# Kernel optimization log

Measured on AMD Instinct MI355X. Metric: run time of the kernel, lower is better.

## Reference

```python
import math
import jax, jax.numpy as jnp
import numpy as np

N_HEADS = 16


def setup_inputs() -> dict:
    key = jax.random.key(0)
    qkv = jax.random.normal(key, (4, 3072, 2048), dtype=jnp.float32)
    return {"qkv": qkv}


def reference(qkv) -> jnp.ndarray:
    bs, width, length = qkv.shape
    assert width % (3 * N_HEADS) == 0
    ch = width // (3 * N_HEADS)
    # [bs*H, 3*ch, T] -> q, k, v each [bs*H, ch, T]
    qkv_r = qkv.reshape(bs * N_HEADS, 3 * ch, length)
    q, k, v = qkv_r[:, :ch], qkv_r[:, ch:2 * ch], qkv_r[:, 2 * ch:]
    scale = 1.0 / math.sqrt(math.sqrt(ch))
    # scores: [bs*H, T, T]
    weight = jnp.einsum('bct,bcs->bts', q * scale, k * scale)
    weight = jax.nn.softmax(weight.astype(jnp.float32), axis=-1).astype(weight.dtype)
    a = jnp.einsum('bts,bcs->bct', weight, v)  # [bs*H, ch, T]
    return a.reshape(bs, N_HEADS * ch, length)
```

## Files before the change

kernel.cpp:

```cpp
#include <hip/hip_runtime.h>
#include <hip/hip_bf16.h>
#include <cstdint>
#include <cstddef>

typedef short bf16x8 __attribute__((ext_vector_type(8)));
typedef float f32x16 __attribute__((ext_vector_type(16)));
typedef unsigned int uint2v __attribute__((ext_vector_type(2)));

#define QSCALE 0.18033688011112043f

__device__ __forceinline__ short f2bf(float f) {
  union { __hip_bfloat16 b; short s; } u;
  u.b = __float2bfloat16(f);
  return u.s;
}

__device__ __forceinline__ float exp2v(float x) {
  float r;
  asm("v_exp_f32 %0, %1" : "=v"(r) : "v"(x));
  return r;
}

__device__ __forceinline__ unsigned int packbf2(float a, float b) {
  union { __hip_bfloat162 h; unsigned int w; } u;
  u.h = __float22bfloat162_rn(float2{a, b});
  return u.w;
}

__device__ __forceinline__ unsigned int fbits(float f) {
  union { float f; unsigned int u; } x; x.f = f; return x.u;
}
__device__ __forceinline__ float bfloat(unsigned int u) {
  union { unsigned int u; float f; } x; x.u = u; return x.f;
}

__device__ __forceinline__ float fmax_x32(float v) {
  const uint2v r = __builtin_amdgcn_permlane32_swap(fbits(v), fbits(v),
                                                    false, false);
  return fmaxf(bfloat(r[0]), bfloat(r[1]));
}
__device__ __forceinline__ float fadd_x32(float v) {
  const uint2v r = __builtin_amdgcn_permlane32_swap(fbits(v), fbits(v),
                                                    false, false);
  return bfloat(r[0]) + bfloat(r[1]);
}

__device__ __forceinline__ void gload16(const short* g, char* l) {
  __builtin_amdgcn_global_load_lds(
      (const __attribute__((address_space(1))) void*)g,
      (__attribute__((address_space(3))) void*)l, 16, 0, 0);
}

__global__ __launch_bounds__(256, 4) void qkv_prep_kernel(
    const float* __restrict__ qkv, short* __restrict__ Kt,
    short* __restrict__ Vb) {
  const int bh = blockIdx.x >> 5;
  const int s0 = (blockIdx.x & 31) << 6;
  const int tid = threadIdx.x;
  const int row = tid >> 2;
  const int part = tid & 3;
  __shared__ float lds[64 * 65];

  const size_t qb = (size_t)bh * (192 * 2048);

  {
    const float* src = qkv + qb + (size_t)(64 + row) * 2048 + s0 + part * 16;
#pragma unroll
    for (int k4 = 0; k4 < 4; ++k4) {
      float4 v = ((const float4*)src)[k4];
      float* p = &lds[row * 65 + part * 16 + k4 * 4];
      p[0] = v.x; p[1] = v.y; p[2] = v.z; p[3] = v.w;
    }
  }
  __syncthreads();
  {
    bf16x8 o0, o1;
#pragma unroll
    for (int k = 0; k < 8; ++k) o0[k] = f2bf(lds[(part * 16 + k) * 65 + row]);
#pragma unroll
    for (int k = 0; k < 8; ++k) o1[k] = f2bf(lds[(part * 16 + 8 + k) * 65 + row]);
    short* dst = Kt + ((size_t)bh * 2048 + s0 + row) * 64 + part * 16;
    *(bf16x8*)dst = o0;
    *(bf16x8*)(dst + 8) = o1;
  }
  {
    const float* src = qkv + qb + (size_t)(128 + row) * 2048 + s0 + part * 16;
    float a[16];
#pragma unroll
    for (int k4 = 0; k4 < 4; ++k4) {
      float4 v = ((const float4*)src)[k4];
      a[k4 * 4 + 0] = v.x; a[k4 * 4 + 1] = v.y;
      a[k4 * 4 + 2] = v.z; a[k4 * 4 + 3] = v.w;
    }
    bf16x8 o0, o1;
#pragma unroll
    for (int k = 0; k < 8; ++k) { o0[k] = f2bf(a[k]); o1[k] = f2bf(a[8 + k]); }
    short* dst = Vb + ((size_t)bh * 64 + row) * 2048 + s0 + part * 16;
    *(bf16x8*)dst = o0;
    *(bf16x8*)(dst + 8) = o1;
  }
}

__global__ __launch_bounds__(512, 4) void attn32_kernel(
    const float* __restrict__ qkv, const short* __restrict__ Kt,
    const short* __restrict__ Vb, float* __restrict__ out) {
  const int bid = blockIdx.x;
  const int vid = (bid & 7) * 64 + (bid >> 3);
  const int bh = vid >> 3;
  const int tblk = vid & 7;
  const int tid = threadIdx.x;
  const int wv = tid >> 6;
  const int lane = tid & 63;
  const int tl = lane & 31;
  const int hi = lane >> 5;
  const int t0w = tblk * 256 + wv * 32;

  __shared__ __align__(16) char smem[32768];

  const size_t qb = (size_t)bh * (192 * 2048);
  bf16x8 qf[4];
#pragma unroll
  for (int kc = 0; kc < 4; ++kc) {
#pragma unroll
    for (int j = 0; j < 8; ++j) {
      const int c = kc * 16 + hi * 8 + j;
      qf[kc][j] = f2bf(qkv[qb + (size_t)c * 2048 + t0w + tl] * QSCALE);
    }
  }

  f32x16 zv;
#pragma unroll
  for (int r = 0; r < 16; ++r) zv[r] = 0.f;

  f32x16 acc[2];
#pragma unroll
  for (int cb = 0; cb < 2; ++cb) acc[cb] = zv;

  float mrun = -1e30f;
  float lsum = 0.f;

  const int rsw = (tl & 7) * 16;
  int off[2][4];
#pragma unroll
  for (int x = 0; x < 2; ++x)
#pragma unroll
    for (int j = 0; j < 4; ++j)
      off[x][j] = (x * 32 + tl) * 128 + ((j * 32 + hi * 16) ^ rsw);

  const int srow = tid >> 3;
  const int sl = tid & 7;
  const short* kg = Kt + (size_t)bh * (2048 * 64) + (size_t)srow * 64 +
                    ((sl ^ (srow & 7)) * 8);
  const short* vg = Vb + ((size_t)bh * 64 + srow) * 2048 +
                    ((sl ^ (srow & 7)) * 8);
  const int ldb = wv * 1024;

  gload16(kg, smem + ldb);
  gload16(vg, smem + 8192 + ldb);

#pragma unroll 2
  for (int ch = 0; ch < 32; ++ch) {
    char* const Kls = smem + (ch & 1) * 16384;
    char* const Vls = Kls + 8192;

    __syncthreads();

    if (ch < 31) {
      char* const Knx = smem + ((ch + 1) & 1) * 16384;
      gload16(kg + (size_t)(ch + 1) * 4096, Knx + ldb);
      gload16(vg + (ch + 1) * 64, Knx + 8192 + ldb);
    }

    f32x16 lg[2];
#pragma unroll
    for (int st = 0; st < 2; ++st) {
      bf16x8 ka = *(const bf16x8*)(Kls + off[st][0]);
      lg[st] = __builtin_amdgcn_mfma_f32_32x32x16_bf16(ka, qf[0], zv, 0, 0, 0);
#pragma unroll
      for (int kc = 1; kc < 4; ++kc) {
        ka = *(const bf16x8*)(Kls + off[st][kc]);
        lg[st] = __builtin_amdgcn_mfma_f32_32x32x16_bf16(ka, qf[kc], lg[st],
                                                         0, 0, 0);
      }
    }

    float w[11];
#pragma unroll
    for (int i = 0; i < 5; ++i)
      w[i] = fmaxf(fmaxf(lg[0][3 * i], lg[0][3 * i + 1]), lg[0][3 * i + 2]);
    w[5] = fmaxf(fmaxf(lg[0][15], lg[1][0]), lg[1][1]);
#pragma unroll
    for (int i = 0; i < 4; ++i)
      w[6 + i] = fmaxf(fmaxf(lg[1][3 * i + 2], lg[1][3 * i + 3]),
                       lg[1][3 * i + 4]);
    w[10] = fmaxf(lg[1][14], lg[1][15]);
    const float x0 = fmaxf(fmaxf(w[0], w[1]), w[2]);
    const float x1 = fmaxf(fmaxf(w[3], w[4]), w[5]);
    const float x2 = fmaxf(fmaxf(w[6], w[7]), w[8]);
    const float x3 = fmaxf(w[9], w[10]);
    float cm = fmax_x32(fmaxf(fmaxf(x0, x1), fmaxf(x2, x3)));
    if (!__all(cm <= mrun + 8.0f)) {
      const float nm = fmaxf(mrun, cm);
      const float fac = exp2v(mrun - nm);
      mrun = nm;
      lsum *= fac;
#pragma unroll
      for (int cb = 0; cb < 2; ++cb)
#pragma unroll
        for (int r = 0; r < 16; ++r) acc[cb][r] *= fac;
    }

    float ps = 0.f;
#pragma unroll
    for (int st = 0; st < 2; ++st) {
#pragma unroll
      for (int r = 0; r < 16; ++r) lg[st][r] = exp2v(lg[st][r] - mrun);
#pragma unroll
      for (int r = 0; r < 8; ++r) ps += lg[st][2 * r] + lg[st][2 * r + 1];
    }
    lsum += ps;

    bf16x8 pa[4];
#pragma unroll
    for (int st = 0; st < 2; ++st) {
#pragma unroll
      for (int kl = 0; kl < 2; ++kl) {
        const unsigned int p0a = packbf2(lg[st][8 * kl + 0], lg[st][8 * kl + 1]);
        const unsigned int p0b = packbf2(lg[st][8 * kl + 2], lg[st][8 * kl + 3]);
        const unsigned int p1a = packbf2(lg[st][8 * kl + 4], lg[st][8 * kl + 5]);
        const unsigned int p1b = packbf2(lg[st][8 * kl + 6], lg[st][8 * kl + 7]);
        const unsigned int sa = hi ? p0a : p1a;
        const unsigned int sb = hi ? p0b : p1b;
        const unsigned int ra = __shfl_xor(sa, 32);
        const unsigned int rb = __shfl_xor(sb, 32);
        union { unsigned int w[4]; bf16x8 v; } u;
        u.w[0] = hi ? ra : p0a;
        u.w[1] = hi ? rb : p0b;
        u.w[2] = hi ? p1a : ra;
        u.w[3] = hi ? p1b : rb;
        pa[st * 2 + kl] = u.v;
      }
    }

#pragma unroll
    for (int cb = 0; cb < 2; ++cb) {
#pragma unroll
      for (int ks = 0; ks < 4; ++ks) {
        const bf16x8 vb = *(const bf16x8*)(Vls + off[cb][ks]);
        acc[cb] = __builtin_amdgcn_mfma_f32_32x32x16_bf16(vb, pa[ks], acc[cb],
                                                          0, 0, 0);
      }
    }
  }

  const float ls = fadd_x32(lsum);
  const float inv = 1.0f / ls;
#pragma unroll
  for (int cb = 0; cb < 2; ++cb) {
#pragma unroll
    for (int r = 0; r < 16; ++r) {
      const int c = cb * 32 + (r & 3) + 8 * (r >> 2) + 4 * hi;
      out[((size_t)bh * 64 + c) * 2048 + t0w + tl] = acc[cb][r] * inv;
    }
  }
}

extern "C" void kernel_launch(void* const* d_in, const int* in_sizes, int n_in,
                              void* d_out, int out_size, void* d_ws,
                              size_t ws_size, hipStream_t stream) {
  (void)in_sizes; (void)n_in; (void)out_size;
  const float* qkv = (const float*)d_in[0];
  float* out = (float*)d_out;
  const size_t kv_elems = (size_t)64 * 2048 * 64;
  if (ws_size < kv_elems * 2 * sizeof(short)) return;
  short* Kt = (short*)d_ws;
  short* Vb = Kt + kv_elems;
  hipLaunchKernelGGL(qkv_prep_kernel, dim3(2048), dim3(256), 0, stream,
                     qkv, Kt, Vb);
  hipLaunchKernelGGL(attn32_kernel, dim3(512), dim3(512), 0, stream,
                     qkv, Kt, Vb, out);
}
```

Baseline: 117.0 us.

## Split each key chunk across wave pairs and merge softmax partials in LDS

Each block now covers 128 query positions instead of 256, and the grid doubles to 1024 blocks. Within each 64-key chunk, a pair of waves splits the keys: each wave does one 32x32 score tile and half of the PV MFMAs. At the end, the two partial online-softmax states (max, sum, accumulator) are combined through LDS before the output is written. This gives more blocks and halves per-wave register state so occupancy can rise (launch bounds raised to 8). The cost is K/V loaded to LDS twice as often per query, plus an extra reduction and barrier in the epilogue.

Result: slower. 309.5 us (+164.6%).

```diff
diff --git a/kernel.cpp b/kernel.cpp
--- a/kernel.cpp
+++ b/kernel.cpp
@@ -101,21 +101,23 @@
   }
 }
 
-__global__ __launch_bounds__(512, 4) void attn32_kernel(
+__global__ __launch_bounds__(512, 8) void attn32_kernel(
     const float* __restrict__ qkv, const short* __restrict__ Kt,
     const short* __restrict__ Vb, float* __restrict__ out) {
   const int bid = blockIdx.x;
-  const int vid = (bid & 7) * 64 + (bid >> 3);
-  const int bh = vid >> 3;
-  const int tblk = vid & 7;
+  const int vid = (bid & 7) * 128 + (bid >> 3);
+  const int bh = vid >> 4;
+  const int tblk = vid & 15;
   const int tid = threadIdx.x;
   const int wv = tid >> 6;
+  const int tt = wv >> 1;
+  const int sh = wv & 1;
   const int lane = tid & 63;
   const int tl = lane & 31;
   const int hi = lane >> 5;
-  const int t0w = tblk * 256 + wv * 32;
-
-  __shared__ __align__(16) char smem[32768];
+  const int t0w = tblk * 128 + tt * 32;
+
+  __shared__ __align__(16) char smem[36864];
 
   const size_t qb = (size_t)bh * (192 * 2048);
   bf16x8 qf[4];
@@ -140,12 +142,16 @@
   float lsum = 0.f;
 
   const int rsw = (tl & 7) * 16;
-  int off[2][4];
-#pragma unroll
-  for (int x = 0; x < 2; ++x)
-#pragma unroll
-    for (int j = 0; j < 4; ++j)
-      off[x][j] = (x * 32 + tl) * 128 + ((j * 32 + hi * 16) ^ rsw);
+  int offk[4], offv[2][2];
+#pragma unroll
+  for (int j = 0; j < 4; ++j)
+    offk[j] = (sh * 32 + tl) * 128 + ((j * 32 + hi * 16) ^ rsw);
+#pragma unroll
+  for (int cb = 0; cb < 2; ++cb)
+#pragma unroll
+    for (int kl = 0; kl < 2; ++kl)
+      offv[cb][kl] = (cb * 32 + tl) * 128 +
+                     ((sh * 64 + kl * 32 + hi * 16) ^ rsw);
 
   const int srow = tid >> 3;
   const int sl = tid & 7;
@@ -171,34 +177,23 @@
       gload16(vg + (ch + 1) * 64, Knx + 8192 + ldb);
     }
 
-    f32x16 lg[2];
-#pragma unroll
-    for (int st = 0; st < 2; ++st) {
-      bf16x8 ka = *(const bf16x8*)(Kls + off[st][0]);
-      lg[st] = __builtin_amdgcn_mfma_f32_32x32x16_bf16(ka, qf[0], zv, 0, 0, 0);
+    f32x16 lg;
+    {
+      bf16x8 ka = *(const bf16x8*)(Kls + offk[0]);
+      lg = __builtin_amdgcn_mfma_f32_32x32x16_bf16(ka, qf[0], zv, 0, 0, 0);
 #pragma unroll
       for (int kc = 1; kc < 4; ++kc) {
-        ka = *(const bf16x8*)(Kls + off[st][kc]);
-        lg[st] = __builtin_amdgcn_mfma_f32_32x32x16_bf16(ka, qf[kc], lg[st],
-                                                         0, 0, 0);
+        ka = *(const bf16x8*)(Kls + offk[kc]);
+        lg = __builtin_amdgcn_mfma_f32_32x32x16_bf16(ka, qf[kc], lg, 0, 0, 0);
       }
     }
 
-    float w[11];
-#pragma unroll
-    for (int i = 0; i < 5; ++i)
-      w[i] = fmaxf(fmaxf(lg[0][3 * i], lg[0][3 * i + 1]), lg[0][3 * i + 2]);
-    w[5] = fmaxf(fmaxf(lg[0][15], lg[1][0]), lg[1][1]);
-#pragma unroll
-    for (int i = 0; i < 4; ++i)
-      w[6 + i] = fmaxf(fmaxf(lg[1][3 * i + 2], lg[1][3 * i + 3]),
-                       lg[1][3 * i + 4]);
-    w[10] = fmaxf(lg[1][14], lg[1][15]);
-    const float x0 = fmaxf(fmaxf(w[0], w[1]), w[2]);
-    const float x1 = fmaxf(fmaxf(w[3], w[4]), w[5]);
-    const float x2 = fmaxf(fmaxf(w[6], w[7]), w[8]);
-    const float x3 = fmaxf(w[9], w[10]);
-    float cm = fmax_x32(fmaxf(fmaxf(x0, x1), fmaxf(x2, x3)));
+    float m8[8];
+#pragma unroll
+    for (int r = 0; r < 8; ++r) m8[r] = fmaxf(lg[r], lg[8 + r]);
+    const float y0 = fmaxf(fmaxf(m8[0], m8[1]), fmaxf(m8[2], m8[3]));
+    const float y1 = fmaxf(fmaxf(m8[4], m8[5]), fmaxf(m8[6], m8[7]));
+    float cm = fmax_x32(fmaxf(y0, y1));
     if (!__all(cm <= mrun + 8.0f)) {
       const float nm = fmaxf(mrun, cm);
       const float fac = exp2v(mrun - nm);
@@ -212,55 +207,74 @@
 
     float ps = 0.f;
 #pragma unroll
-    for (int st = 0; st < 2; ++st) {
-#pragma unroll
-      for (int r = 0; r < 16; ++r) lg[st][r] = exp2v(lg[st][r] - mrun);
-#pragma unroll
-      for (int r = 0; r < 8; ++r) ps += lg[st][2 * r] + lg[st][2 * r + 1];
-    }
+    for (int r = 0; r < 16; ++r) lg[r] = exp2v(lg[r] - mrun);
+#pragma unroll
+    for (int r = 0; r < 8; ++r) ps += lg[2 * r] + lg[2 * r + 1];
     lsum += ps;
 
-    bf16x8 pa[4];
-#pragma unroll
-    for (int st = 0; st < 2; ++st) {
+    bf16x8 pa[2];
+#pragma unroll
+    for (int kl = 0; kl < 2; ++kl) {
+      const unsigned int p0a = packbf2(lg[8 * kl + 0], lg[8 * kl + 1]);
+      const unsigned int p0b = packbf2(lg[8 * kl + 2], lg[8 * kl + 3]);
+      const unsigned int p1a = packbf2(lg[8 * kl + 4], lg[8 * kl + 5]);
+      const unsigned int p1b = packbf2(lg[8 * kl + 6], lg[8 * kl + 7]);
+      const unsigned int sa = hi ? p0a : p1a;
+      const unsigned int sb = hi ? p0b : p1b;
+      const unsigned int ra = __shfl_xor(sa, 32);
+      const unsigned int rb = __shfl_xor(sb, 32);
+      union { unsigned int w[4]; bf16x8 v; } u;
+      u.w[0] = hi ? ra : p0a;
+      u.w[1] = hi ? rb : p0b;
+      u.w[2] = hi ? p1a : ra;
+      u.w[3] = hi ? p1b : rb;
+      pa[kl] = u.v;
+    }
+
+#pragma unroll
+    for (int cb = 0; cb < 2; ++cb) {
 #pragma unroll
       for (int kl = 0; kl < 2; ++kl) {
-        const unsigned int p0a = packbf2(lg[st][8 * kl + 0], lg[st][8 * kl + 1]);
-        const unsigned int p0b = packbf2(lg[st][8 * kl + 2], lg[st][8 * kl + 3]);
-        const unsigned int p1a = packbf2(lg[st][8 * kl + 4], lg[st][8 * kl + 5]);
-        const unsigned int p1b = packbf2(lg[st][8 * kl + 6], lg[st][8 * kl + 7]);
-        const unsigned int sa = hi ? p0a : p1a;
-        const unsigned int sb = hi ? p0b : p1b;
-        const unsigned int ra = __shfl_xor(sa, 32);
-        const unsigned int rb = __shfl_xor(sb, 32);
-        union { unsigned int w[4]; bf16x8 v; } u;
-        u.w[0] = hi ? ra : p0a;
-        u.w[1] = hi ? rb : p0b;
-        u.w[2] = hi ? p1a : ra;
-        u.w[3] = hi ? p1b : rb;
-        pa[st * 2 + kl] = u.v;
-      }
-    }
-
-#pragma unroll
-    for (int cb = 0; cb < 2; ++cb) {
-#pragma unroll
-      for (int ks = 0; ks < 4; ++ks) {
-        const bf16x8 vb = *(const bf16x8*)(Vls + off[cb][ks]);
-        acc[cb] = __builtin_amdgcn_mfma_f32_32x32x16_bf16(vb, pa[ks], acc[cb],
+        const bf16x8 vb = *(const bf16x8*)(Vls + offv[cb][kl]);
+        acc[cb] = __builtin_amdgcn_mfma_f32_32x32x16_bf16(vb, pa[kl], acc[cb],
                                                           0, 0, 0);
       }
     }
   }
 
-  const float ls = fadd_x32(lsum);
-  const float inv = 1.0f / ls;
-#pragma unroll
-  for (int cb = 0; cb < 2; ++cb) {
-#pragma unroll
-    for (int r = 0; r < 16; ++r) {
-      const int c = cb * 32 + (r & 3) + 8 * (r >> 2) + 4 * hi;
-      out[((size_t)bh * 64 + c) * 2048 + t0w + tl] = acc[cb][r] * inv;
+  __syncthreads();
+  float* const accb = (float*)smem;
+  float* const mlb = (float*)(smem + 32768);
+  if (sh == 1) {
+    float* ap = accb + (tt * 64 + lane) * 32;
+    union { f32x16 v; float4 q[4]; } u;
+#pragma unroll
+    for (int cb = 0; cb < 2; ++cb) {
+      u.v = acc[cb];
+#pragma unroll
+      for (int i = 0; i < 4; ++i) ((float4*)ap)[cb * 4 + i] = u.q[i];
+    }
+    mlb[(tt * 64 + lane) * 2 + 0] = mrun;
+    mlb[(tt * 64 + lane) * 2 + 1] = lsum;
+  }
+  __syncthreads();
+  if (sh == 0) {
+    const float m1 = mlb[(tt * 64 + lane) * 2 + 0];
+    const float l1 = mlb[(tt * 64 + lane) * 2 + 1];
+    const float m = fmaxf(mrun, m1);
+    const float f0 = exp2v(mrun - m);
+    const float f1 = exp2v(m1 - m);
+    const float ls = fadd_x32(lsum * f0 + l1 * f1);
+    const float inv = 1.0f / ls;
+    const float* ap = accb + (tt * 64 + lane) * 32;
+#pragma unroll
+    for (int cb = 0; cb < 2; ++cb) {
+#pragma unroll
+      for (int r = 0; r < 16; ++r) {
+        const int c = cb * 32 + (r & 3) + 8 * (r >> 2) + 4 * hi;
+        const float o = (acc[cb][r] * f0 + ap[cb * 16 + r] * f1) * inv;
+        out[((size_t)bh * 64 + c) * 2048 + t0w + tl] = o;
+      }
     }
   }
 }
@@ -277,6 +291,6 @@
   short* Vb = Kt + kv_elems;
   hipLaunchKernelGGL(qkv_prep_kernel, dim3(2048), dim3(256), 0, stream,
                      qkv, Kt, Vb);
-  hipLaunchKernelGGL(attn32_kernel, dim3(512), dim3(512), 0, stream,
+  hipLaunchKernelGGL(attn32_kernel, dim3(1024), dim3(512), 0, stream,
                      qkv, Kt, Vb, out);
 }
```
